# Performance work log

Hardware: AMD Instinct MI355X
Metric: run time of the kernel (lower is better)

## Reference

```python
import jax, jax.numpy as jnp
import numpy as np

N = 150000      # nodes
E_AST = 300000  # ast edges
E_CFG = 250000  # cfg edges
D = 256         # in_size = out_size
N_STEPS = 2


def _gru(a, h, Wih, Whh, bih, bhh):
    # torch.nn.GRUCell semantics: input a, hidden h
    gi = a @ Wih.T + bih            # [N, 3D]
    gh = h @ Whh.T + bhh            # [N, 3D]
    ir, iz, i_n = jnp.split(gi, 3, axis=-1)
    hr, hz, h_n = jnp.split(gh, 3, axis=-1)
    r = jax.nn.sigmoid(ir + hr)
    z = jax.nn.sigmoid(iz + hz)
    n = jnp.tanh(i_n + r * h_n)
    return (1.0 - z) * n + z * h


def _gated_graph_conv(h, src, dst, W, b, Wih, Whh, bih, bhh):
    # DGL GatedGraphConv, n_etypes=1, in_feats == out_feats
    n_nodes = h.shape[0]
    for _ in range(N_STEPS):
        m = (h @ W.T + b)[src]                                   # per-edge gather [E, D]
        a = jax.ops.segment_sum(m, dst, num_segments=n_nodes)    # scatter-sum to dst
        h = _gru(a, h, Wih, Whh, bih, bhh)
    return h


def setup_inputs() -> dict:
    key = jax.random.key(0)
    ks = jax.random.split(key, 16)
    s = 1.0 / np.sqrt(D)
    inp = {
        'nodes': jax.random.normal(ks[0], (N, D), jnp.float32),
        'ast_src': jax.random.randint(ks[1], (E_AST,), 0, N),
        'ast_dst': jax.random.randint(ks[2], (E_AST,), 0, N),
        'cfg_src': jax.random.randint(ks[3], (E_CFG,), 0, N),
        'cfg_dst': jax.random.randint(ks[4], (E_CFG,), 0, N),
        'W_ast': jax.random.normal(ks[5], (D, D), jnp.float32) * s,
        'b_ast': jnp.zeros((D,), jnp.float32),
        'Wih_ast': jax.random.normal(ks[6], (3 * D, D), jnp.float32) * s,
        'Whh_ast': jax.random.normal(ks[7], (3 * D, D), jnp.float32) * s,
        'bih_ast': jnp.zeros((3 * D,), jnp.float32),
        'bhh_ast': jnp.zeros((3 * D,), jnp.float32),
        'w1': jax.random.normal(ks[8], (D, 2 * D), jnp.float32) * (1.0 / np.sqrt(2 * D)),
        'b1': jnp.zeros((D,), jnp.float32),
        'W_cpg': jax.random.normal(ks[9], (D, D), jnp.float32) * s,
        'b_cpg': jnp.zeros((D,), jnp.float32),
        'Wih_cpg': jax.random.normal(ks[10], (3 * D, D), jnp.float32) * s,
        'Whh_cpg': jax.random.normal(ks[11], (3 * D, D), jnp.float32) * s,
        'bih_cpg': jnp.zeros((3 * D,), jnp.float32),
        'bhh_cpg': jnp.zeros((3 * D,), jnp.float32),
        'w2': jax.random.normal(ks[12], (D, 2 * D), jnp.float32) * (1.0 / np.sqrt(2 * D)),
        'b2': jnp.zeros((D,), jnp.float32),
    }
    return inp


def reference(nodes, ast_src, ast_dst, cfg_src, cfg_dst,
              W_ast, b_ast, Wih_ast, Whh_ast, bih_ast, bhh_ast,
              w1, b1,
              W_cpg, b_cpg, Wih_cpg, Whh_cpg, bih_cpg, bhh_cpg,
              w2, b2):
    # ast branch: GatedGraphConv -> concat with input -> fn_1
    h_ast = _gated_graph_conv(nodes, ast_src, ast_dst,
                              W_ast, b_ast, Wih_ast, Whh_ast, bih_ast, bhh_ast)
    hiddens = jnp.concatenate([h_ast, nodes], axis=-1) @ w1.T + b1   # [N, D]
    # cpg branch: GatedGraphConv -> concat with hiddens -> fn_2
    h_cpg = _gated_graph_conv(hiddens, cfg_src, cfg_dst,
                              W_cpg, b_cpg, Wih_cpg, Whh_cpg, bih_cpg, bhh_cpg)
    logits = jnp.concatenate([h_cpg, hiddens], axis=-1) @ w2.T + b2  # [N, D]
    return logits
```

## Files before the change

kernel.cpp:

```cpp
#include <hip/hip_runtime.h>

typedef _Float16 f16;
typedef _Float16 f16x8 __attribute__((ext_vector_type(8)));
typedef float f32x16 __attribute__((ext_vector_type(16)));

__device__ __forceinline__ f16x8 cvt8p(const float* p) {
  float4 a = *(const float4*)p;
  float4 b = *(const float4*)(p + 4);
  f16x8 v;
  v[0] = (f16)a.x; v[1] = (f16)a.y; v[2] = (f16)a.z; v[3] = (f16)a.w;
  v[4] = (f16)b.x; v[5] = (f16)b.y; v[6] = (f16)b.z; v[7] = (f16)b.w;
  return v;
}

__device__ __forceinline__ void gload16(const void* g, void* l) {
  __builtin_amdgcn_global_load_lds((const __attribute__((address_space(1))) unsigned int*)g,
                                   (__attribute__((address_space(3))) unsigned int*)l, 16, 0, 0);
}

__device__ __forceinline__ float sigm(float x) {
  return __builtin_amdgcn_rcpf(1.f + __expf(-x));
}
__device__ __forceinline__ float tanh_(float x) {
  x = fminf(15.f, fmaxf(-15.f, x));
  float e = __expf(2.f * x);
  return 1.f - 2.f * __builtin_amdgcn_rcpf(e + 1.f);
}


__global__ void k_cvt8(const float* __restrict__ x, f16* __restrict__ y, long n) {
  long i = ((long)blockIdx.x * blockDim.x + threadIdx.x) * 8;
  long stride = (long)gridDim.x * blockDim.x * 8;
  for (; i < n; i += stride) *(f16x8*)(y + i) = cvt8p(x + i);
}

__global__ void k_wc2(const float* __restrict__ Wih, const float* __restrict__ W,
                      unsigned char* __restrict__ dstb) {
  int j = blockIdx.x;
  int k = threadIdx.x;
  float s = 0.f;
  for (int c = 0; c < 256; ++c) s = fmaf(Wih[j * 256 + c], W[c * 256 + k], s);
  int g = j >> 8, hcol = j & 255;
  int hb = hcol >> 5, trow = hcol & 31;
  int kc = k >> 6, kl = k & 63;
  int slot = (kl >> 3) ^ (trow & 7);
  size_t byte = (size_t)hb * 98304 + (size_t)kc * 12288 +
                (size_t)(g * 32 + trow) * 128 + slot * 16 + (kl & 7) * 2;
  *(f16*)(dstb + byte) = (f16)s;
}

__global__ void k_whh2(const float* __restrict__ Whh, unsigned char* __restrict__ dstb) {
  int j = blockIdx.x;
  int k = threadIdx.x;
  float s = Whh[j * 256 + k];
  int g = j >> 8, hcol = j & 255;
  int hb = hcol >> 5, trow = hcol & 31;
  int kc = 4 + (k >> 6), kl = k & 63;
  int slot = (kl >> 3) ^ (trow & 7);
  size_t byte = (size_t)hb * 98304 + (size_t)kc * 12288 +
                (size_t)(g * 32 + trow) * 128 + slot * 16 + (kl & 7) * 2;
  *(f16*)(dstb + byte) = (f16)s;
}

__global__ void k_prepw(const float* __restrict__ w, unsigned char* __restrict__ dstb) {
  int j = blockIdx.x;
  int cg = j >> 6, R = j & 63;
  for (int k = threadIdx.x; k < 512; k += 256) {
    int kc = k >> 6, kl = k & 63;
    int slot = (kl >> 3) ^ (R & 7);
    size_t byte = (size_t)(cg * 8 + kc) * 8192 + (size_t)R * 128 + slot * 16 + (kl & 7) * 2;
    *(f16*)(dstb + byte) = (f16)w[j * 512 + k];
  }
}

__global__ void k_v(const float* __restrict__ Wih, const float* __restrict__ b,
                    float* __restrict__ v) {
  int j = blockIdx.x * blockDim.x + threadIdx.x;
  if (j < 768) {
    float s = 0.f;
    for (int c = 0; c < 256; ++c) s = fmaf(Wih[j * 256 + c], b[c], s);
    v[j] = s;
  }
}

__global__ void k_hist(const int* __restrict__ dst, int* __restrict__ cnt, int E) {
  int e = blockIdx.x * 256 + threadIdx.x;
  if (e < E) atomicAdd(&cnt[dst[e]], 1);
}

__global__ void k_scan1(const int* __restrict__ deg, int* __restrict__ rowptr,
                        int* __restrict__ bsum, int n) {
  __shared__ int buf[256];
  int i = blockIdx.x * 256 + threadIdx.x;
  int v = (i < n) ? deg[i] : 0;
  buf[threadIdx.x] = v;
  __syncthreads();
  for (int off = 1; off < 256; off <<= 1) {
    int t = 0;
    if ((int)threadIdx.x >= off) t = buf[threadIdx.x - off];
    __syncthreads();
    buf[threadIdx.x] += t;
    __syncthreads();
  }
  if (i < n) rowptr[i] = buf[threadIdx.x] - v;
  if (threadIdx.x == 255) bsum[blockIdx.x] = buf[255];
}

__global__ void k_scan2(int* __restrict__ bsum, int nb) {
  __shared__ int buf[1024];
  int v = ((int)threadIdx.x < nb) ? bsum[threadIdx.x] : 0;
  buf[threadIdx.x] = v;
  __syncthreads();
  for (int off = 1; off < 1024; off <<= 1) {
    int t = 0;
    if ((int)threadIdx.x >= off) t = buf[threadIdx.x - off];
    __syncthreads();
    buf[threadIdx.x] += t;
    __syncthreads();
  }
  if ((int)threadIdx.x < nb) bsum[threadIdx.x] = buf[threadIdx.x] - v;
}

__global__ void k_scan3(int* __restrict__ rowptr, const int* __restrict__ bsum,
                        int n, int E) {
  int i = blockIdx.x * 256 + threadIdx.x;
  if (i < n) rowptr[i] += bsum[blockIdx.x];
  if (i == n) rowptr[n] = E;
}

__global__ void k_fill(const int* __restrict__ src, const int* __restrict__ dst,
                       const int* __restrict__ rowptr, int* __restrict__ cnt,
                       int* __restrict__ esrc, int E) {
  int e = blockIdx.x * 256 + threadIdx.x;
  if (e < E) {
    int d = dst[e];
    int r = atomicAdd(&cnt[d], 1);
    esrc[rowptr[d] + r] = src[e];
  }
}

__global__ void k_gather(const f16* __restrict__ h, const int* __restrict__ rowptr,
                         const int* __restrict__ esrc, f16* __restrict__ ag, int n) {
  int g = threadIdx.x >> 5, l = threadIdx.x & 31;
  int node = blockIdx.x * 8 + g;
  if (node >= n) return;
  int e0 = rowptr[node], e1 = rowptr[node + 1];
  float acc[8];
#pragma unroll
  for (int j = 0; j < 8; ++j) acc[j] = 0.f;
  int e = e0;
  for (; e + 2 <= e1; e += 2) {
    int s0 = esrc[e], s1 = esrc[e + 1];
    f16x8 hv0 = *(const f16x8*)(h + (long)s0 * 256 + l * 8);
    f16x8 hv1 = *(const f16x8*)(h + (long)s1 * 256 + l * 8);
#pragma unroll
    for (int j = 0; j < 8; ++j) acc[j] += (float)hv0[j] + (float)hv1[j];
  }
  if (e < e1) {
    int s0 = esrc[e];
    f16x8 hv0 = *(const f16x8*)(h + (long)s0 * 256 + l * 8);
#pragma unroll
    for (int j = 0; j < 8; ++j) acc[j] += (float)hv0[j];
  }
  f16x8 o;
#pragma unroll
  for (int j = 0; j < 8; ++j) o[j] = (f16)acc[j];
  *(f16x8*)(ag + (long)node * 256 + l * 8) = o;
}

__global__ __launch_bounds__(256, 4) void k_gru(
    const f16* __restrict__ ag, const f16* __restrict__ hin,
    const unsigned char* __restrict__ wprep, const float* __restrict__ bih,
    const float* __restrict__ bhh, const float* __restrict__ vv,
    const int* __restrict__ rowptr, f16* __restrict__ hout, int n, int nper) {
  __shared__ unsigned char SM[24576 + 512];
  float* Ds = (float*)(SM + 24576);
  int bid = blockIdx.x;
  int w = (bid & 7) * nper + (bid >> 3);
  int rt = w >> 3, hb = w & 7;
  int row0 = rt * 128;
  int tid = threadIdx.x, lane = tid & 63, wid = tid >> 6;
  int l31 = lane & 31, hi = lane >> 5;
  const unsigned char* wb = wprep + (size_t)hb * 98304;

  auto stage = [&](int c, unsigned char* dst) {
    const unsigned char* s0 = wb + (size_t)c * 12288;
#pragma unroll
    for (int i = 0; i < 3; ++i) {
      int r = i * 4 + wid;
      gload16(s0 + r * 1024 + lane * 16, dst + r * 1024);
    }
  };

  int arow = row0 + wid * 32 + l31;
  const f16* agp = ag + (size_t)arow * 256 + hi * 8;
  const f16* hp = hin + (size_t)arow * 256 + hi * 8;

  f16x8 a[4];
  auto loadA = [&](const f16* p, int koff) {
#pragma unroll
    for (int ks = 0; ks < 4; ++ks)
      a[ks] = *(const f16x8*)(p + koff + ks * 16);
  };
  int sl0 = l31 & 7;
  auto runC = [&](const unsigned char* Bb, f32x16& aR, f32x16& aZ, f32x16& aN) {
#pragma unroll
    for (int ks = 0; ks < 4; ++ks) {
      int sl = (ks * 2 + hi) ^ sl0;
      const unsigned char* base = Bb + sl * 16;
      f16x8 b0 = *(const f16x8*)(base + (0 * 32 + l31) * 128);
      aR = __builtin_amdgcn_mfma_f32_32x32x16_f16(a[ks], b0, aR, 0, 0, 0);
      f16x8 b1 = *(const f16x8*)(base + (1 * 32 + l31) * 128);
      aZ = __builtin_amdgcn_mfma_f32_32x32x16_f16(a[ks], b1, aZ, 0, 0, 0);
      f16x8 b2 = *(const f16x8*)(base + (2 * 32 + l31) * 128);
      aN = __builtin_amdgcn_mfma_f32_32x32x16_f16(a[ks], b2, aN, 0, 0, 0);
    }
  };

  f32x16 accR, accZ, accNI, accNH;
#pragma unroll
  for (int j = 0; j < 16; ++j) { accR[j] = 0.f; accZ[j] = 0.f; accNI[j] = 0.f; accNH[j] = 0.f; }

  stage(0, SM);
  loadA(agp, 0);
  if (tid < 128) {
    int grow = row0 + tid;
    Ds[tid] = (grow < n) ? (float)(rowptr[grow + 1] - rowptr[grow]) : 0.f;
  }
  __syncthreads();

  stage(1, SM + 12288);
  runC(SM, accR, accZ, accNI);
  loadA(agp, 64);
  __syncthreads();
  stage(2, SM);
  runC(SM + 12288, accR, accZ, accNI);
  loadA(agp, 128);
  __syncthreads();
  stage(3, SM + 12288);
  runC(SM, accR, accZ, accNI);
  loadA(agp, 192);
  __syncthreads();
  stage(4, SM);
  runC(SM + 12288, accR, accZ, accNI);
  loadA(hp, 0);
  __syncthreads();
  stage(5, SM + 12288);
  runC(SM, accR, accZ, accNH);
  loadA(hp, 64);
  __syncthreads();
  stage(6, SM);
  runC(SM + 12288, accR, accZ, accNH);
  loadA(hp, 128);
  __syncthreads();
  stage(7, SM + 12288);
  runC(SM, accR, accZ, accNH);
  loadA(hp, 192);
  __syncthreads();
  runC(SM + 12288, accR, accZ, accNH);

  int gcol = hb * 32 + l31;
  float br = bih[gcol] + bhh[gcol];
  float bz = bih[256 + gcol] + bhh[256 + gcol];
  float bi_n = bih[512 + gcol], bh_n = bhh[512 + gcol];
  float vr = vv[gcol], vz = vv[256 + gcol], vn = vv[512 + gcol];
  int wrow = wid * 32;

#pragma unroll
  for (int rg = 0; rg < 16; ++rg) {
    int crow = (rg & 3) + 8 * (rg >> 2) + 4 * hi;
    int grow = row0 + wrow + crow;
    float dg = Ds[wrow + crow];
    float hold = (float)hin[(size_t)grow * 256 + gcol];
    float r = sigm(accR[rg] + br + dg * vr);
    float z = sigm(accZ[rg] + bz + dg * vz);
    float nn = tanh_(accNI[rg] + bi_n + dg * vn + r * (accNH[rg] + bh_n));
    if (grow < n)
      hout[(size_t)grow * 256 + gcol] = (f16)((1.f - z) * nn + z * hold);
  }
}

template <int WMODE>
__global__ __launch_bounds__(256, 4) void k_fn(
    const f16* __restrict__ hb, const f16* __restrict__ base16,
    const unsigned char* __restrict__ wp, const float* __restrict__ bias,
    float* __restrict__ out32, f16* __restrict__ out16, int n, int nper) {
  __shared__ unsigned char SM[16384];
  int bid = blockIdx.x;
  int w = (bid & 7) * nper + (bid >> 3);
  int rt = w >> 2, cg = w & 3;
  int row0 = rt * 128;
  int tid = threadIdx.x, lane = tid & 63, wid = tid >> 6;
  int l31 = lane & 31, hi = lane >> 5;
  const unsigned char* wb = wp + (size_t)cg * 65536;

  auto stage = [&](int c, unsigned char* dst) {
    const unsigned char* s0 = wb + (size_t)c * 8192;
#pragma unroll
    for (int i = 0; i < 2; ++i) {
      int r = i * 4 + wid;
      gload16(s0 + r * 1024 + lane * 16, dst + r * 1024);
    }
  };

  int arow = row0 + wid * 32 + l31;
  const f16* hbp = hb + (size_t)arow * 256 + hi * 8;
  const f16* bsp = base16 + (size_t)arow * 256 + hi * 8;

  f16x8 a[4];
  auto loadA = [&](const f16* p, int koff) {
#pragma unroll
    for (int ks = 0; ks < 4; ++ks)
      a[ks] = *(const f16x8*)(p + koff + ks * 16);
  };
  int sl0 = l31 & 7;

  f32x16 acc0, acc1;
#pragma unroll
  for (int j = 0; j < 16; ++j) { acc0[j] = 0.f; acc1[j] = 0.f; }

  auto runC = [&](const unsigned char* Bb) {
#pragma unroll
    for (int ks = 0; ks < 4; ++ks) {
      int sl = (ks * 2 + hi) ^ sl0;
      const unsigned char* base = Bb + sl * 16;
      f16x8 b0 = *(const f16x8*)(base + (0 + l31) * 128);
      acc0 = __builtin_amdgcn_mfma_f32_32x32x16_f16(a[ks], b0, acc0, 0, 0, 0);
      f16x8 b1 = *(const f16x8*)(base + (32 + l31) * 128);
      acc1 = __builtin_amdgcn_mfma_f32_32x32x16_f16(a[ks], b1, acc1, 0, 0, 0);
    }
  };

  stage(0, SM);
  loadA(hbp, 0);
  __syncthreads();
  stage(1, SM + 8192); runC(SM);        loadA(hbp, 64);  __syncthreads();
  stage(2, SM);        runC(SM + 8192); loadA(hbp, 128); __syncthreads();
  stage(3, SM + 8192); runC(SM);        loadA(hbp, 192); __syncthreads();
  stage(4, SM);        runC(SM + 8192); loadA(bsp, 0);   __syncthreads();
  stage(5, SM + 8192); runC(SM);        loadA(bsp, 64);  __syncthreads();
  stage(6, SM);        runC(SM + 8192); loadA(bsp, 128); __syncthreads();
  stage(7, SM + 8192); runC(SM);        loadA(bsp, 192); __syncthreads();
  runC(SM + 8192);

  int colb = cg * 64;
  float bb0 = bias[colb + l31], bb1 = bias[colb + 32 + l31];
#pragma unroll
  for (int rg = 0; rg < 16; ++rg) {
    int grow = row0 + wid * 32 + (rg & 3) + 8 * (rg >> 2) + 4 * hi;
    if (grow < n) {
      if (WMODE == 0) {
        out32[(size_t)grow * 256 + colb + l31] = acc0[rg] + bb0;
        out32[(size_t)grow * 256 + colb + 32 + l31] = acc1[rg] + bb1;
      } else {
        out16[(size_t)grow * 256 + colb + l31] = (f16)(acc0[rg] + bb0);
        out16[(size_t)grow * 256 + colb + 32 + l31] = (f16)(acc1[rg] + bb1);
      }
    }
  }
}

extern "C" void kernel_launch(void* const* d_in, const int* in_sizes, int n_in,
                              void* d_out, int out_size, void* d_ws, size_t ws_size,
                              hipStream_t stream) {
  const float* nodes = (const float*)d_in[0];
  const int* asrc = (const int*)d_in[1];
  const int* adst = (const int*)d_in[2];
  const int* csrc = (const int*)d_in[3];
  const int* cdst = (const int*)d_in[4];
  const float* W_ast = (const float*)d_in[5];
  const float* b_ast = (const float*)d_in[6];
  const float* Wih_a = (const float*)d_in[7];
  const float* Whh_a = (const float*)d_in[8];
  const float* bih_a = (const float*)d_in[9];
  const float* bhh_a = (const float*)d_in[10];
  const float* w1 = (const float*)d_in[11];
  const float* b1 = (const float*)d_in[12];
  const float* W_cpg = (const float*)d_in[13];
  const float* b_cpg = (const float*)d_in[14];
  const float* Wih_c = (const float*)d_in[15];
  const float* Whh_c = (const float*)d_in[16];
  const float* bih_c = (const float*)d_in[17];
  const float* bhh_c = (const float*)d_in[18];
  const float* w2 = (const float*)d_in[19];
  const float* b2 = (const float*)d_in[20];
  float* out = (float*)d_out;

  const int N = in_sizes[0] / 256;
  const int EA = in_sizes[1];
  const int EC = in_sizes[3];
  const long ND = (long)N * 256;

  char* ws = (char*)d_ws;
  size_t off = 0;
  auto carve = [&](size_t bytes) -> char* {
    char* p = ws + off;
    off += (bytes + 255) & ~(size_t)255;
    return p;
  };
  f16* h0 = (f16*)carve(ND * 2);
  f16* h1 = (f16*)carve(ND * 2);
  f16* ag = (f16*)carve(ND * 2);
  f16* nd16 = (f16*)carve(ND * 2);
  unsigned char* wpA = (unsigned char*)carve(786432);
  unsigned char* wpC = (unsigned char*)carve(786432);
  unsigned char* w1p = (unsigned char*)carve(262144);
  unsigned char* w2p = (unsigned char*)carve(262144);
  float* vA = (float*)carve(768 * 4);
  float* vC = (float*)carve(768 * 4);
  int* rowptr = (int*)carve((size_t)(N + 1) * 4);
  int* cnt = (int*)carve((size_t)N * 4);
  int* esrc = (int*)carve((size_t)(EA > EC ? EA : EC) * 4);
  int* bsum = (int*)carve(1024 * 4);
  (void)ws_size; (void)n_in; (void)out_size;

  const int NRB = (N + 127) / 128;
  const int GGRID = NRB * 8;
  const int FGRID = NRB * 4;
  const int SBLK = (N + 255) / 256;
  {
    int blocks = (int)((ND / 8 + 255) / 256);
    if (blocks > 2048) blocks = 2048;
    k_cvt8<<<blocks, 256, 0, stream>>>(nodes, nd16, ND);
  }

  k_wc2<<<768, 256, 0, stream>>>(Wih_a, W_ast, wpA);
  k_wc2<<<768, 256, 0, stream>>>(Wih_c, W_cpg, wpC);
  k_whh2<<<768, 256, 0, stream>>>(Whh_a, wpA);
  k_whh2<<<768, 256, 0, stream>>>(Whh_c, wpC);
  k_prepw<<<256, 256, 0, stream>>>(w1, w1p);
  k_prepw<<<256, 256, 0, stream>>>(w2, w2p);
  k_v<<<3, 256, 0, stream>>>(Wih_a, b_ast, vA);
  k_v<<<3, 256, 0, stream>>>(Wih_c, b_cpg, vC);

  auto run_branch = [&](const int* src, const int* dst, int E, const unsigned char* wprep,
                        const float* bih, const float* bhh, const float* v,
                        const f16* hstart, f16* t1, f16* t2) {
    hipMemsetAsync(cnt, 0, (size_t)N * 4, stream);
    k_hist<<<(E + 255) / 256, 256, 0, stream>>>(dst, cnt, E);
    k_scan1<<<SBLK, 256, 0, stream>>>(cnt, rowptr, bsum, N);
    k_scan2<<<1, 1024, 0, stream>>>(bsum, SBLK);
    k_scan3<<<SBLK, 256, 0, stream>>>(rowptr, bsum, N, E);
    hipMemsetAsync(cnt, 0, (size_t)N * 4, stream);
    k_fill<<<(E + 255) / 256, 256, 0, stream>>>(src, dst, rowptr, cnt, esrc, E);
    k_gather<<<(N + 7) / 8, 256, 0, stream>>>(hstart, rowptr, esrc, ag, N);
    k_gru<<<GGRID, 256, 0, stream>>>(ag, hstart, wprep, bih, bhh, v, rowptr, t1, N, NRB);
    k_gather<<<(N + 7) / 8, 256, 0, stream>>>(t1, rowptr, esrc, ag, N);
    k_gru<<<GGRID, 256, 0, stream>>>(ag, t1, wprep, bih, bhh, v, rowptr, t2, N, NRB);
  };

  run_branch(asrc, adst, EA, wpA, bih_a, bhh_a, vA, nd16, h1, h0);
  k_fn<1><<<FGRID, 256, 0, stream>>>(h0, nd16, w1p, b1, nullptr, h1, N, FGRID / 8);
  run_branch(csrc, cdst, EC, wpC, bih_c, bhh_c, vC, h1, h0, nd16);
  k_fn<0><<<FGRID, 256, 0, stream>>>(nd16, h1, w2p, b2, out, nullptr, N, FGRID / 8);
}
```

Baseline: 1.311 ms.

## Precombine GRU biases, reuse histogram counts for CSR fill, raise GRU occupancy

Measured after the change: 1.513 ms. +15.4%, slower.

```diff
diff --git a/kernel.cpp b/kernel.cpp
--- a/kernel.cpp
+++ b/kernel.cpp
@@ -73,14 +73,24 @@
   }
 }
 
-__global__ void k_v(const float* __restrict__ Wih, const float* __restrict__ b,
-                    float* __restrict__ v) {
-  int j = blockIdx.x * blockDim.x + threadIdx.x;
-  if (j < 768) {
-    float s = 0.f;
-    for (int c = 0; c < 256; ++c) s = fmaf(Wih[j * 256 + c], b[c], s);
-    v[j] = s;
-  }
+__global__ void k_bias(const float* __restrict__ Wih, const float* __restrict__ b,
+                       const float* __restrict__ bih, const float* __restrict__ bhh,
+                       float* __restrict__ B7) {
+  int j = threadIdx.x;
+  float vr = 0.f, vz = 0.f, vn = 0.f;
+  for (int c = 0; c < 256; ++c) {
+    float bc = b[c];
+    vr = fmaf(Wih[(size_t)j * 256 + c], bc, vr);
+    vz = fmaf(Wih[(size_t)(256 + j) * 256 + c], bc, vz);
+    vn = fmaf(Wih[(size_t)(512 + j) * 256 + c], bc, vn);
+  }
+  B7[j] = bih[j] + bhh[j];
+  B7[256 + j] = bih[256 + j] + bhh[256 + j];
+  B7[512 + j] = bih[512 + j];
+  B7[768 + j] = bhh[512 + j];
+  B7[1024 + j] = vr;
+  B7[1280 + j] = vz;
+  B7[1536 + j] = vn;
 }
 
 __global__ void k_hist(const int* __restrict__ dst, int* __restrict__ cnt, int E) {
@@ -134,8 +144,8 @@
   int e = blockIdx.x * 256 + threadIdx.x;
   if (e < E) {
     int d = dst[e];
-    int r = atomicAdd(&cnt[d], 1);
-    esrc[rowptr[d] + r] = src[e];
+    int r = atomicSub(&cnt[d], 1);
+    esrc[rowptr[d] + r - 1] = src[e];
   }
 }
 
@@ -168,10 +178,9 @@
   *(f16x8*)(ag + (long)node * 256 + l * 8) = o;
 }
 
-__global__ __launch_bounds__(256, 4) void k_gru(
+__global__ __launch_bounds__(256, 5) void k_gru(
     const f16* __restrict__ ag, const f16* __restrict__ hin,
-    const unsigned char* __restrict__ wprep, const float* __restrict__ bih,
-    const float* __restrict__ bhh, const float* __restrict__ vv,
+    const unsigned char* __restrict__ wprep, const float* __restrict__ B7,
     const int* __restrict__ rowptr, f16* __restrict__ hout, int n, int nper) {
   __shared__ unsigned char SM[24576 + 512];
   float* Ds = (float*)(SM + 24576);
@@ -260,10 +269,10 @@
   runC(SM + 12288, accR, accZ, accNH);
 
   int gcol = hb * 32 + l31;
-  float br = bih[gcol] + bhh[gcol];
-  float bz = bih[256 + gcol] + bhh[256 + gcol];
-  float bi_n = bih[512 + gcol], bh_n = bhh[512 + gcol];
-  float vr = vv[gcol], vz = vv[256 + gcol], vn = vv[512 + gcol];
+  float br = B7[gcol];
+  float bz = B7[256 + gcol];
+  float bi_n = B7[512 + gcol], bh_n = B7[768 + gcol];
+  float vr = B7[1024 + gcol], vz = B7[1280 + gcol], vn = B7[1536 + gcol];
   int wrow = wid * 32;
 
 #pragma unroll
@@ -406,8 +415,8 @@
   unsigned char* wpC = (unsigned char*)carve(786432);
   unsigned char* w1p = (unsigned char*)carve(262144);
   unsigned char* w2p = (unsigned char*)carve(262144);
-  float* vA = (float*)carve(768 * 4);
-  float* vC = (float*)carve(768 * 4);
+  float* B7A = (float*)carve(1792 * 4);
+  float* B7C = (float*)carve(1792 * 4);
   int* rowptr = (int*)carve((size_t)(N + 1) * 4);
   int* cnt = (int*)carve((size_t)N * 4);
   int* esrc = (int*)carve((size_t)(EA > EC ? EA : EC) * 4);
@@ -430,27 +439,25 @@
   k_whh2<<<768, 256, 0, stream>>>(Whh_c, wpC);
   k_prepw<<<256, 256, 0, stream>>>(w1, w1p);
   k_prepw<<<256, 256, 0, stream>>>(w2, w2p);
-  k_v<<<3, 256, 0, stream>>>(Wih_a, b_ast, vA);
-  k_v<<<3, 256, 0, stream>>>(Wih_c, b_cpg, vC);
+  k_bias<<<1, 256, 0, stream>>>(Wih_a, b_ast, bih_a, bhh_a, B7A);
+  k_bias<<<1, 256, 0, stream>>>(Wih_c, b_cpg, bih_c, bhh_c, B7C);
+  hipMemsetAsync(cnt, 0, (size_t)N * 4, stream);
 
   auto run_branch = [&](const int* src, const int* dst, int E, const unsigned char* wprep,
-                        const float* bih, const float* bhh, const float* v,
-                        const f16* hstart, f16* t1, f16* t2) {
-    hipMemsetAsync(cnt, 0, (size_t)N * 4, stream);
+                        const float* B7, const f16* hstart, f16* t1, f16* t2) {
     k_hist<<<(E + 255) / 256, 256, 0, stream>>>(dst, cnt, E);
     k_scan1<<<SBLK, 256, 0, stream>>>(cnt, rowptr, bsum, N);
     k_scan2<<<1, 1024, 0, stream>>>(bsum, SBLK);
     k_scan3<<<SBLK, 256, 0, stream>>>(rowptr, bsum, N, E);
-    hipMemsetAsync(cnt, 0, (size_t)N * 4, stream);
     k_fill<<<(E + 255) / 256, 256, 0, stream>>>(src, dst, rowptr, cnt, esrc, E);
     k_gather<<<(N + 7) / 8, 256, 0, stream>>>(hstart, rowptr, esrc, ag, N);
-    k_gru<<<GGRID, 256, 0, stream>>>(ag, hstart, wprep, bih, bhh, v, rowptr, t1, N, NRB);
+    k_gru<<<GGRID, 256, 0, stream>>>(ag, hstart, wprep, B7, rowptr, t1, N, NRB);
     k_gather<<<(N + 7) / 8, 256, 0, stream>>>(t1, rowptr, esrc, ag, N);
-    k_gru<<<GGRID, 256, 0, stream>>>(ag, t1, wprep, bih, bhh, v, rowptr, t2, N, NRB);
-  };
-
-  run_branch(asrc, adst, EA, wpA, bih_a, bhh_a, vA, nd16, h1, h0);
+    k_gru<<<GGRID, 256, 0, stream>>>(ag, t1, wprep, B7, rowptr, t2, N, NRB);
+  };
+
+  run_branch(asrc, adst, EA, wpA, B7A, nd16, h1, h0);
   k_fn<1><<<FGRID, 256, 0, stream>>>(h0, nd16, w1p, b1, nullptr, h1, N, FGRID / 8);
-  run_branch(csrc, cdst, EC, wpC, bih_c, bhh_c, vC, h1, h0, nd16);
+  run_branch(csrc, cdst, EC, wpC, B7C, h1, h0, nd16);
   k_fn<0><<<FGRID, 256, 0, stream>>>(nd16, h1, w2p, b2, out, nullptr, N, FGRID / 8);
 }
```
